# Optimization experiments

Measured on AMD Instinct MI355X. Metric: run time of the kernel, lower is better.

## Reference

```python
import jax, jax.numpy as jnp
import numpy as np

B, C_IN, T_IN = 128, 128, 2500
C_OUT, K, STRIDE, PAD = 64, 27, 4, 13  # T_out = 625
BN_EPS = 1e-5
SURROGATE_ALPHA = 4.0


def binarize_weight(w):
    """1-bit (XNOR-Net style) weight quantization with straight-through estimator.
    w: (O, I, K). Per-output-channel scale = mean |w|."""
    alpha = jnp.mean(jnp.abs(w), axis=(1, 2), keepdims=True)
    wq = jnp.sign(w) * alpha
    return w + jax.lax.stop_gradient(wq - w)


def spike(x):
    """Heaviside spike with sigmoid surrogate gradient (STE)."""
    hard = (x > 0).astype(x.dtype)
    soft = jax.nn.sigmoid(SURROGATE_ALPHA * x)
    return soft + jax.lax.stop_gradient(hard - soft)


def setup_inputs() -> dict:
    key = jax.random.key(0)
    ks = jax.random.split(key, 8)
    scale_conv = 1.0 / np.sqrt(C_IN * K)
    scale_lin = 1.0 / np.sqrt(C_OUT)
    return {
        "x": jax.random.normal(ks[0], (B, C_IN, T_IN), dtype=jnp.float32),
        "conv_w": jax.random.normal(ks[1], (C_OUT, C_IN, K), dtype=jnp.float32) * scale_conv,
        "conv_b": jnp.zeros((C_OUT,), dtype=jnp.float32),
        "bn_gamma": jnp.ones((C_OUT,), dtype=jnp.float32),
        "bn_beta": jnp.zeros((C_OUT,), dtype=jnp.float32),
        "bn_mean": jax.random.normal(ks[2], (C_OUT,), dtype=jnp.float32) * 0.1,
        "bn_var": jax.random.uniform(ks[3], (C_OUT,), dtype=jnp.float32, minval=0.5, maxval=1.5),
        "wq": jax.random.normal(ks[4], (C_OUT, C_OUT), dtype=jnp.float32) * scale_lin,
        "wk": jax.random.normal(ks[5], (C_OUT, C_OUT), dtype=jnp.float32) * scale_lin,
        "wv": jax.random.normal(ks[6], (C_OUT, C_OUT), dtype=jnp.float32) * scale_lin,
        "wo": jax.random.normal(ks[7], (C_OUT, C_OUT), dtype=jnp.float32) * scale_lin,
    }


def reference(x, conv_w, conv_b, bn_gamma, bn_beta, bn_mean, bn_var, wq, wk, wv, wo):
    # --- 1-bit quantized conv1d, stride 4 ---
    w_bin = binarize_weight(conv_w)
    y = jax.lax.conv_general_dilated(
        x, w_bin, window_strides=(STRIDE,), padding=[(PAD, PAD)],
        dimension_numbers=("NCH", "OIH", "NCH"))
    y = y + conv_b[None, :, None]  # (B, C_OUT, 625)

    # --- BatchNorm1d (inference stats) + ELU ---
    inv = jax.lax.rsqrt(bn_var + BN_EPS)
    y = (y - bn_mean[None, :, None]) * (inv * bn_gamma)[None, :, None] + bn_beta[None, :, None]
    y = jax.nn.elu(y)

    # --- Global spiking attention (single head) ---
    s = spike(y)                                   # (B, C, T) binary spikes
    q = jnp.einsum("oc,bct->bot", wq, s)           # (B, C, T)
    k = jnp.einsum("oc,bct->bot", wk, s)
    v = jnp.einsum("oc,bct->bot", wv, y)
    scores = jnp.einsum("bct,bcs->bts", q, k) / jnp.sqrt(jnp.asarray(C_OUT, y.dtype))
    attn = jax.nn.softmax(scores, axis=-1)         # (B, T, T)
    ctx = jnp.einsum("bts,bcs->bct", attn, v)      # (B, C, T)
    out = y + jnp.einsum("oc,bct->bot", wo, ctx)   # residual
    return out
```

## Files before the change

### kernel.cpp

```cpp
#include <hip/hip_runtime.h>
#include <math.h>

#define B_    128
#define CIN   128
#define TIN   2500
#define COUT  64
#define KW    27
#define TOUT  625
#define TPAD  640
#define CTT   32
#define GROWS 152

typedef __bf16 bf16x8 __attribute__((ext_vector_type(8)));
typedef float  f32x4  __attribute__((ext_vector_type(4)));

__device__ __forceinline__ unsigned short f32_to_bf16_rne(float v) {
    unsigned u = __float_as_uint(v);
    u += 0x7FFFu + ((u >> 16) & 1u);
    return (unsigned short)(u >> 16);
}

__device__ __forceinline__ f32x4 mfma_bf16(bf16x8 a, bf16x8 b, f32x4 c) {
    return __builtin_amdgcn_mfma_f32_16x16x32_bf16(a, b, c, 0, 0, 0);
}

__global__ void binarize_kernel(const float* __restrict__ w,
                                unsigned* __restrict__ sgn2,
                                float* __restrict__ alpha_out) {
    int o = blockIdx.x, tid = threadIdx.x;
    __shared__ float red[256];
    const float* wo_ = w + (size_t)o * (CIN * KW);
    float s = 0.f;
    for (int idx = tid; idx < CIN * KW; idx += 256) s += fabsf(wo_[idx]);
    red[tid] = s;
    __syncthreads();
    for (int st = 128; st > 0; st >>= 1) {
        if (tid < st) red[tid] += red[tid + st];
        __syncthreads();
    }
    if (tid == 0) alpha_out[o] = red[0] / (float)(CIN * KW);

    for (int t = tid; t < KW * 4; t += 256) {
        int kk = t >> 2, kg = t & 3;
        unsigned u = 0;
#pragma unroll
        for (int cs = 0; cs < 4; cs++) {
#pragma unroll
            for (int j = 0; j < 8; j++) {
                int c = cs * 32 + kg * 8 + j;
                float v = wo_[c * KW + kk];
                unsigned bit = (v > 0.f) ? 0u : 1u;
                u |= bit << (cs * 8 + j);
            }
        }
        sgn2[(kk * 4 + kg) * 64 + o] = u;
    }
}

__global__ void transpose_w_kernel(const float* __restrict__ wq, const float* __restrict__ wk,
                                   const float* __restrict__ wv, const float* __restrict__ wo,
                                   const float* __restrict__ conv_b, const float* __restrict__ gamma_,
                                   const float* __restrict__ beta_, const float* __restrict__ mean_,
                                   const float* __restrict__ var_, const float* __restrict__ alpha_,
                                   unsigned short* __restrict__ w3_h, unsigned short* __restrict__ w3_l,
                                   unsigned short* __restrict__ wo_h, unsigned short* __restrict__ wo_l,
                                   float* __restrict__ scA, float* __restrict__ scB) {
    if (blockIdx.x < 3) {
        const float* srcs[3] = {wq, wk, wv};
        const float* src = srcs[blockIdx.x];
        unsigned short* dh = w3_h + (size_t)blockIdx.x * 4096;
        unsigned short* dl = w3_l + (size_t)blockIdx.x * 4096;
        for (int idx = threadIdx.x; idx < 4096; idx += 256) {
            float v = src[idx];
            unsigned short h = f32_to_bf16_rne(v);
            float hf = __uint_as_float((unsigned)h << 16);
            dh[idx] = h;
            dl[idx] = f32_to_bf16_rne(v - hf);
        }
    } else if (blockIdx.x == 3) {
        for (int idx = threadIdx.x; idx < 4096; idx += 256) {
            float v = wo[idx];
            unsigned short h = f32_to_bf16_rne(v);
            float hf = __uint_as_float((unsigned)h << 16);
            wo_h[idx] = h;
            wo_l[idx] = f32_to_bf16_rne(v - hf);
        }
    } else {
        int o = threadIdx.x;
        if (o < 64) {
            float inv = rsqrtf(var_[o] + 1e-5f);
            float G = gamma_[o] * inv;
            scA[o] = alpha_[o] * G;
            scB[o] = (conv_b[o] - mean_[o]) * G + beta_[o];
        }
    }
}

__global__ __launch_bounds__(256, 4) void conv_kernel(
    const float* __restrict__ x, const unsigned* __restrict__ sgn2,
    const float* __restrict__ scA, const float* __restrict__ scB,
    const unsigned short* __restrict__ w3_h, const unsigned short* __restrict__ w3_l,
    float* __restrict__ y_out,
    unsigned short* __restrict__ q_h, unsigned short* __restrict__ k_h,
    unsigned short* __restrict__ vT_h)
{
    __shared__ __align__(16) unsigned short xhi[GROWS * 128];
    __shared__ __align__(16) unsigned long long sgnlut[16];
    unsigned short* y_sh = xhi;
    unsigned short* s_sh = xhi + 2048;
    unsigned short* q_sh = xhi + 4096;
    unsigned short* k_sh = xhi + 6144;
    unsigned short* v_sh = xhi + 8192;

    int b = blockIdx.y;
    int t0 = blockIdx.x * CTT;
    int tid = threadIdx.x;

    if (tid < 16) {
        unsigned long long e = 0;
#pragma unroll
        for (int j = 0; j < 4; ++j) {
            unsigned long long h = ((tid >> j) & 1) ? 0xBF80ull : 0x3F80ull;
            e |= h << (16 * j);
        }
        sgnlut[tid] = e;
    }

    const float* xb = x + (size_t)b * CIN * TIN;
    int gbase = 4 * t0 - 13;
    for (int task = tid; task < 16 * GROWS; task += 256) {
        int c8 = task / GROWS, gl = task - c8 * GROWS;
        int g = gbase + gl;
        bool valid = (gl < 151) && ((unsigned)g < (unsigned)TIN);
        float vs[8];
#pragma unroll
        for (int j = 0; j < 8; j++)
            vs[j] = valid ? xb[(size_t)(c8 * 8 + j) * TIN + g] : 0.f;
        union { unsigned u[4]; uint4 q; } H;
#pragma unroll
        for (int j = 0; j < 4; j++) {
            unsigned short h0 = f32_to_bf16_rne(vs[2 * j]);
            unsigned short h1 = f32_to_bf16_rne(vs[2 * j + 1]);
            H.u[j] = (unsigned)h0 | ((unsigned)h1 << 16);
        }
        int c8p = c8 ^ ((gl >> 2) & 15);
        *(uint4*)(xhi + gl * 128 + c8p * 8) = H.q;
    }
    __syncthreads();

    int wave = tid >> 6, lane = tid & 63;
    int o0 = wave * 16;
    int n = lane & 15, kg = lane >> 4;

    f32x4 acc0 = {0.f, 0.f, 0.f, 0.f};
    f32x4 acc1 = {0.f, 0.f, 0.f, 0.f};

    const unsigned* sgb = sgn2 + (size_t)kg * 64 + o0 + n;
    unsigned sa = sgb[0];

#pragma unroll 1
    for (int kk = 0; kk < KW; ++kk) {
        unsigned na = 0;
        if (kk < KW - 1) na = sgb[(kk + 1) * 256];
        int gl = 4 * n + kk;
        int rot = (gl >> 2) & 15;
        const unsigned short* xr0 = xhi + gl * 128;
        const unsigned short* xr1 = xr0 + 8192;
#pragma unroll
        for (int cs = 0; cs < 4; ++cs) {
            int c8p = (cs * 4 + kg) ^ rot;
            bf16x8 b0 = *(const bf16x8*)(xr0 + c8p * 8);
            bf16x8 b1 = *(const bf16x8*)(xr1 + c8p * 8);
            unsigned byte = (sa >> (8 * cs)) & 0xFFu;
            union { unsigned long long u[2]; bf16x8 v; } A;
            A.u[0] = sgnlut[byte & 15u];
            A.u[1] = sgnlut[byte >> 4];
            acc0 = mfma_bf16(A.v, b0, acc0);
            acc1 = mfma_bf16(A.v, b1, acc1);
        }
        sa = na;
    }

    int quad = kg, col = n;
    unsigned long long ypk[2], spk[2];
#pragma unroll
    for (int tt = 0; tt < 2; ++tt) {
        int t_g = t0 + tt * 16 + col;
        f32x4 a = tt ? acc1 : acc0;
        unsigned long long yp = 0, sp = 0;
#pragma unroll
        for (int r = 0; r < 4; ++r) {
            int o = o0 + quad * 4 + r;
            float s = a[r] * scA[o] + scB[o];
            float yv = s > 0.f ? s : expm1f(s);
            if (t_g < TOUT) {
                y_out[((size_t)b * COUT + o) * TOUT + t_g] = yv;
                yp |= (unsigned long long)f32_to_bf16_rne(yv) << (16 * r);
                if (yv > 0.f) sp |= 0x3F80ull << (16 * r);
            }
        }
        ypk[tt] = yp; spk[tt] = sp;
    }
    __syncthreads();

    int c8w = (o0 >> 3) + (quad >> 1);
    int cof = (quad & 1) * 4;
#pragma unroll
    for (int tt = 0; tt < 2; ++tt) {
        int tl = tt * 16 + col;
        int idx = tl * 64 + ((c8w ^ (tl & 7)) << 3) + cof;
        *(unsigned long long*)(y_sh + idx) = ypk[tt];
        *(unsigned long long*)(s_sh + idx) = spk[tt];
    }
    __syncthreads();

    bf16x8 sf[2][2], yf[2][2];
#pragma unroll
    for (int tt = 0; tt < 2; ++tt)
#pragma unroll
        for (int ks = 0; ks < 2; ++ks) {
            int tl = tt * 16 + col;
            int idx = tl * 64 + (((ks * 4 + quad) ^ (tl & 7)) << 3);
            sf[tt][ks] = *(const bf16x8*)(s_sh + idx);
            yf[tt][ks] = *(const bf16x8*)(y_sh + idx);
        }
    size_t wofs = (size_t)(o0 + col) * 64 + quad * 8;
    f32x4 qa[2], ka[2], va[2];
#pragma unroll
    for (int tt = 0; tt < 2; ++tt) {
        qa[tt] = (f32x4){0.f, 0.f, 0.f, 0.f};
        ka[tt] = (f32x4){0.f, 0.f, 0.f, 0.f};
        va[tt] = (f32x4){0.f, 0.f, 0.f, 0.f};
    }
#pragma unroll
    for (int ks = 0; ks < 2; ++ks) {
        bf16x8 aqh = *(const bf16x8*)(w3_h + wofs + ks * 32);
        bf16x8 aql = *(const bf16x8*)(w3_l + wofs + ks * 32);
        bf16x8 akh = *(const bf16x8*)(w3_h + 4096 + wofs + ks * 32);
        bf16x8 akl = *(const bf16x8*)(w3_l + 4096 + wofs + ks * 32);
        bf16x8 avh = *(const bf16x8*)(w3_h + 8192 + wofs + ks * 32);
        bf16x8 avl = *(const bf16x8*)(w3_l + 8192 + wofs + ks * 32);
#pragma unroll
        for (int tt = 0; tt < 2; ++tt) {
            qa[tt] = mfma_bf16(aqh, sf[tt][ks], qa[tt]);
            qa[tt] = mfma_bf16(aql, sf[tt][ks], qa[tt]);
            ka[tt] = mfma_bf16(akh, sf[tt][ks], ka[tt]);
            ka[tt] = mfma_bf16(akl, sf[tt][ks], ka[tt]);
            va[tt] = mfma_bf16(avh, yf[tt][ks], va[tt]);
            va[tt] = mfma_bf16(avl, yf[tt][ks], va[tt]);
        }
    }
#pragma unroll
    for (int tt = 0; tt < 2; ++tt) {
        int tl = tt * 16 + col;
        int idx = tl * 64 + ((c8w ^ (tl & 7)) << 3) + cof;
        unsigned long long qp = 0, kp = 0;
#pragma unroll
        for (int r = 0; r < 4; ++r) {
            qp |= (unsigned long long)f32_to_bf16_rne(qa[tt][r]) << (16 * r);
            kp |= (unsigned long long)f32_to_bf16_rne(ka[tt][r]) << (16 * r);
        }
        *(unsigned long long*)(q_sh + idx) = qp;
        *(unsigned long long*)(k_sh + idx) = kp;
#pragma unroll
        for (int r = 0; r < 4; ++r) {
            int c = o0 + quad * 4 + r;
            int vidx = c * 32 + (((tt * 2 + (col >> 3)) ^ quad) << 3) + (col & 7);
            v_sh[vidx] = f32_to_bf16_rne(va[tt][r]);
        }
    }
    __syncthreads();

    {
        int tl = tid >> 3, seg = tid & 7;
        int idx = tl * 64 + ((seg ^ (tl & 7)) << 3);
        uint4 qv = *(const uint4*)(q_sh + idx);
        uint4 kv = *(const uint4*)(k_sh + idx);
        size_t go = ((size_t)b * TPAD + t0 + tl) * 64 + seg * 8;
        *(uint4*)(q_h + go) = qv;
        *(uint4*)(k_h + go) = kv;
        int c = tid >> 2, ts = tid & 3;
        int vidx = c * 32 + ((ts ^ ((c >> 2) & 3)) << 3);
        uint4 vv = *(const uint4*)(v_sh + vidx);
        *(uint4*)(vT_h + ((size_t)b * 64 + c) * TPAD + t0 + ts * 8) = vv;
    }
}

__global__ __launch_bounds__(512, 3) void attn_kernel(
    const unsigned short* __restrict__ q_h, const unsigned short* __restrict__ k_h,
    const unsigned short* __restrict__ vT_h, const float* __restrict__ y,
    const unsigned short* __restrict__ wo_h, const unsigned short* __restrict__ wo_l,
    float* __restrict__ out)
{
    __shared__ __align__(16) float sc_sh[16 * 648];
    __shared__ float ctx_sh[2 * 64 * 17];
    __shared__ float rden[16];

    int b = blockIdx.y, t0 = blockIdx.x * 16, tid = threadIdx.x;
    int wave = tid >> 6, lane = tid & 63;
    int quad = lane >> 4, nlo = lane & 15;

    const unsigned short* qb = q_h + ((size_t)b * TPAD + t0 + nlo) * 64 + quad * 8;
    bf16x8 qa0 = *(const bf16x8*)(qb);
    bf16x8 qa1 = *(const bf16x8*)(qb + 32);
    const unsigned short* kbase = k_h + (size_t)b * TPAD * 64 + quad * 8;
#pragma unroll 5
    for (int nt = 0; nt < 5; ++nt) {
        int s = wave * 80 + nt * 16 + nlo;
        const unsigned short* krow = kbase + (size_t)s * 64;
        bf16x8 kb0 = *(const bf16x8*)(krow);
        bf16x8 kb1 = *(const bf16x8*)(krow + 32);
        f32x4 acc = {0.f, 0.f, 0.f, 0.f};
        acc = mfma_bf16(qa0, kb0, acc);
        acc = mfma_bf16(qa1, kb1, acc);
#pragma unroll
        for (int r = 0; r < 4; ++r)
            sc_sh[(quad * 4 + r) * 648 + s] = acc[r] * 0.125f;
    }
    __syncthreads();

    int ti1 = tid >> 5, sg = tid & 31;
    float* srow = &sc_sh[ti1 * 648];
    float mx = -3.0e38f;
    for (int s = sg; s < TOUT; s += 32) mx = fmaxf(mx, srow[s]);
#pragma unroll
    for (int off = 16; off >= 1; off >>= 1) mx = fmaxf(mx, __shfl_xor(mx, off));

    unsigned short* prow = (unsigned short*)srow;
    float sum = 0.f;
#pragma unroll
    for (int k2 = 0; k2 < 10; ++k2) {
        int s = 2 * sg + 64 * k2;
        float2 v2 = *(const float2*)(srow + s);
        float e0 = (s     < TOUT) ? __expf(v2.x - mx) : 0.f;
        float e1 = (s + 1 < TOUT) ? __expf(v2.y - mx) : 0.f;
        sum += e0 + e1;
        unsigned u0 = __float_as_uint(e0); u0 += 0x7FFFu + ((u0 >> 16) & 1u);
        unsigned u1 = __float_as_uint(e1); u1 += 0x7FFFu + ((u1 >> 16) & 1u);
        *(unsigned*)(prow + s) = (u0 >> 16) | (u1 & 0xFFFF0000u);
    }
#pragma unroll
    for (int off = 16; off >= 1; off >>= 1) sum += __shfl_xor(sum, off);
    if (sg == 0) rden[ti1] = 1.f / sum;
    __syncthreads();

    int cw = (wave & 3) * 16, kh = wave >> 2;
    const unsigned short* vb = vT_h + ((size_t)b * 64 + cw + nlo) * TPAD;
    const unsigned short* pb = (const unsigned short*)sc_sh + nlo * 1296;
    f32x4 cacc = {0.f, 0.f, 0.f, 0.f};
    int ks0 = kh * 10;
#pragma unroll 5
    for (int i = 0; i < 10; ++i) {
        int ks = ks0 + i;
        bf16x8 pv = *(const bf16x8*)(pb + ks * 32 + quad * 8);
        bf16x8 v8 = *(const bf16x8*)(vb + ks * 32 + quad * 8);
        cacc = mfma_bf16(pv, v8, cacc);
    }
#pragma unroll
    for (int r = 0; r < 4; ++r)
        ctx_sh[kh * 1088 + (cw + nlo) * 17 + quad * 4 + r] = cacc[r] * rden[quad * 4 + r];
    __syncthreads();

    if (wave < 4) {
        const unsigned short* woh = wo_h + (size_t)(wave * 16 + nlo) * 64 + quad * 8;
        const unsigned short* wol = wo_l + (size_t)(wave * 16 + nlo) * 64 + quad * 8;
        f32x4 oacc = {0.f, 0.f, 0.f, 0.f};
#pragma unroll
        for (int ks = 0; ks < 2; ++ks) {
            union { unsigned short u[8]; bf16x8 v; } Bc;
#pragma unroll
            for (int j = 0; j < 8; ++j) {
                int c = ks * 32 + quad * 8 + j;
                float cv = ctx_sh[c * 17 + nlo] + ctx_sh[1088 + c * 17 + nlo];
                Bc.u[j] = f32_to_bf16_rne(cv);
            }
            bf16x8 ah = *(const bf16x8*)(woh + ks * 32);
            bf16x8 al = *(const bf16x8*)(wol + ks * 32);
            oacc = mfma_bf16(ah, Bc.v, oacc);
            oacc = mfma_bf16(al, Bc.v, oacc);
        }
        int t_g = t0 + nlo;
        if (t_g < TOUT) {
#pragma unroll
            for (int r = 0; r < 4; ++r) {
                int o = wave * 16 + quad * 4 + r;
                size_t off = ((size_t)b * COUT + o) * TOUT + t_g;
                out[off] = y[off] + oacc[r];
            }
        }
    }
}

extern "C" void kernel_launch(void* const* d_in, const int* in_sizes, int n_in,
                              void* d_out, int out_size, void* d_ws, size_t ws_size,
                              hipStream_t stream) {
    const float* x        = (const float*)d_in[0];
    const float* conv_w   = (const float*)d_in[1];
    const float* conv_b   = (const float*)d_in[2];
    const float* bn_gamma = (const float*)d_in[3];
    const float* bn_beta  = (const float*)d_in[4];
    const float* bn_mean  = (const float*)d_in[5];
    const float* bn_var   = (const float*)d_in[6];
    const float* wq       = (const float*)d_in[7];
    const float* wk       = (const float*)d_in[8];
    const float* wv       = (const float*)d_in[9];
    const float* wo       = (const float*)d_in[10];
    float* out = (float*)d_out;
    float* ws  = (float*)d_ws;

    unsigned* sgn2        = (unsigned*)ws;
    float* alpha          = ws + 110592;
    float* scA            = ws + 110656;
    float* scB            = ws + 110720;
    unsigned short* w3_h  = (unsigned short*)(ws + 110848);
    unsigned short* w3_l  = (unsigned short*)(ws + 116992);
    unsigned short* wo_h  = (unsigned short*)(ws + 123136);
    unsigned short* wo_l  = (unsigned short*)(ws + 125184);
    float* yb             = ws + 131072;
    unsigned short* q_h   = (unsigned short*)(ws + 5251072);
    unsigned short* k_h   = (unsigned short*)(ws + 7872512);
    unsigned short* vT_h  = (unsigned short*)(ws + 10493952);

    hipLaunchKernelGGL(binarize_kernel, dim3(64), dim3(256), 0, stream, conv_w, sgn2, alpha);
    hipLaunchKernelGGL(transpose_w_kernel, dim3(5), dim3(256), 0, stream,
                       wq, wk, wv, wo, conv_b, bn_gamma, bn_beta, bn_mean, bn_var, alpha,
                       w3_h, w3_l, wo_h, wo_l, scA, scB);
    hipLaunchKernelGGL(conv_kernel, dim3(20, 128), dim3(256), 0, stream,
                       x, sgn2, scA, scB, w3_h, w3_l, yb, q_h, k_h, vT_h);
    hipLaunchKernelGGL(attn_kernel, dim3(40, 128), dim3(512), 0, stream,
                       q_h, k_h, vT_h, yb, wo_h, wo_l, out);
}
```

Baseline: 433.0 us.

## Merge prep kernels, use 32x32 MFMA conv with split-K, remap blocks for XCD locality

Merges the binarize and weight-transpose kernels into one prep kernel, removing a launch and the alpha round trip through memory. The conv kernel now uses 32x32x16 bf16 MFMA, with the channel dimension split across wave pairs and partial sums reduced through shared memory. Both conv and attention blocks get a swizzled block-id mapping (id&7 stride) so neighbouring tiles of the same batch land on the same XCD for cache locality. This adds an extra LDS reduction and barrier in the conv epilogue, and leaves half the waves idle during it.

```diff
diff --git a/kernel.cpp b/kernel.cpp
--- a/kernel.cpp
+++ b/kernel.cpp
@@ -13,6 +13,7 @@
 
 typedef __bf16 bf16x8 __attribute__((ext_vector_type(8)));
 typedef float  f32x4  __attribute__((ext_vector_type(4)));
+typedef float  f32x16 __attribute__((ext_vector_type(16)));
 
 __device__ __forceinline__ unsigned short f32_to_bf16_rne(float v) {
     unsigned u = __float_as_uint(v);
@@ -24,74 +25,69 @@
     return __builtin_amdgcn_mfma_f32_16x16x32_bf16(a, b, c, 0, 0, 0);
 }
 
-__global__ void binarize_kernel(const float* __restrict__ w,
-                                unsigned* __restrict__ sgn2,
-                                float* __restrict__ alpha_out) {
-    int o = blockIdx.x, tid = threadIdx.x;
-    __shared__ float red[256];
-    const float* wo_ = w + (size_t)o * (CIN * KW);
-    float s = 0.f;
-    for (int idx = tid; idx < CIN * KW; idx += 256) s += fabsf(wo_[idx]);
-    red[tid] = s;
-    __syncthreads();
-    for (int st = 128; st > 0; st >>= 1) {
-        if (tid < st) red[tid] += red[tid + st];
+__global__ void prep_kernel(const float* __restrict__ w,
+                            const float* __restrict__ wq, const float* __restrict__ wk,
+                            const float* __restrict__ wv, const float* __restrict__ wo,
+                            const float* __restrict__ conv_b, const float* __restrict__ gamma_,
+                            const float* __restrict__ beta_, const float* __restrict__ mean_,
+                            const float* __restrict__ var_,
+                            unsigned* __restrict__ sgn2,
+                            unsigned short* __restrict__ w3_h, unsigned short* __restrict__ w3_l,
+                            unsigned short* __restrict__ wo_h, unsigned short* __restrict__ wo_l,
+                            float* __restrict__ scA, float* __restrict__ scB) {
+    int blk = blockIdx.x, tid = threadIdx.x;
+    if (blk < 64) {
+        __shared__ float red[256];
+        const float* wrow = w + (size_t)blk * (CIN * KW);
+        float s = 0.f;
+        for (int idx = tid; idx < CIN * KW; idx += 256) s += fabsf(wrow[idx]);
+        red[tid] = s;
         __syncthreads();
-    }
-    if (tid == 0) alpha_out[o] = red[0] / (float)(CIN * KW);
-
-    for (int t = tid; t < KW * 4; t += 256) {
-        int kk = t >> 2, kg = t & 3;
-        unsigned u = 0;
-#pragma unroll
-        for (int cs = 0; cs < 4; cs++) {
-#pragma unroll
-            for (int j = 0; j < 8; j++) {
-                int c = cs * 32 + kg * 8 + j;
-                float v = wo_[c * KW + kk];
-                unsigned bit = (v > 0.f) ? 0u : 1u;
-                u |= bit << (cs * 8 + j);
+        for (int st = 128; st > 0; st >>= 1) {
+            if (tid < st) red[tid] += red[tid + st];
+            __syncthreads();
+        }
+        if (tid == 0) {
+            float alpha = red[0] / (float)(CIN * KW);
+            float inv = rsqrtf(var_[blk] + 1e-5f);
+            float G = gamma_[blk] * inv;
+            scA[blk] = alpha * G;
+            scB[blk] = (conv_b[blk] - mean_[blk]) * G + beta_[blk];
+        }
+        for (int t = tid; t < KW * 4; t += 256) {
+            int kk = t >> 2, kg = t & 3;
+            unsigned u = 0;
+#pragma unroll
+            for (int cs = 0; cs < 4; cs++) {
+#pragma unroll
+                for (int j = 0; j < 8; j++) {
+                    int c = cs * 32 + kg * 8 + j;
+                    float v = wrow[c * KW + kk];
+                    unsigned bit = (v > 0.f) ? 0u : 1u;
+                    u |= bit << (cs * 8 + j);
+                }
             }
-        }
-        sgn2[(kk * 4 + kg) * 64 + o] = u;
-    }
-}
-
-__global__ void transpose_w_kernel(const float* __restrict__ wq, const float* __restrict__ wk,
-                                   const float* __restrict__ wv, const float* __restrict__ wo,
-                                   const float* __restrict__ conv_b, const float* __restrict__ gamma_,
-                                   const float* __restrict__ beta_, const float* __restrict__ mean_,
-                                   const float* __restrict__ var_, const float* __restrict__ alpha_,
-                                   unsigned short* __restrict__ w3_h, unsigned short* __restrict__ w3_l,
-                                   unsigned short* __restrict__ wo_h, unsigned short* __restrict__ wo_l,
-                                   float* __restrict__ scA, float* __restrict__ scB) {
-    if (blockIdx.x < 3) {
+            sgn2[(kk * 4 + kg) * 64 + blk] = u;
+        }
+    } else if (blk < 67) {
         const float* srcs[3] = {wq, wk, wv};
-        const float* src = srcs[blockIdx.x];
-        unsigned short* dh = w3_h + (size_t)blockIdx.x * 4096;
-        unsigned short* dl = w3_l + (size_t)blockIdx.x * 4096;
-        for (int idx = threadIdx.x; idx < 4096; idx += 256) {
+        const float* src = srcs[blk - 64];
+        unsigned short* dh = w3_h + (size_t)(blk - 64) * 4096;
+        unsigned short* dl = w3_l + (size_t)(blk - 64) * 4096;
+        for (int idx = tid; idx < 4096; idx += 256) {
             float v = src[idx];
             unsigned short h = f32_to_bf16_rne(v);
             float hf = __uint_as_float((unsigned)h << 16);
             dh[idx] = h;
             dl[idx] = f32_to_bf16_rne(v - hf);
         }
-    } else if (blockIdx.x == 3) {
-        for (int idx = threadIdx.x; idx < 4096; idx += 256) {
+    } else {
+        for (int idx = tid; idx < 4096; idx += 256) {
             float v = wo[idx];
             unsigned short h = f32_to_bf16_rne(v);
             float hf = __uint_as_float((unsigned)h << 16);
             wo_h[idx] = h;
             wo_l[idx] = f32_to_bf16_rne(v - hf);
-        }
-    } else {
-        int o = threadIdx.x;
-        if (o < 64) {
-            float inv = rsqrtf(var_[o] + 1e-5f);
-            float G = gamma_[o] * inv;
-            scA[o] = alpha_[o] * G;
-            scB[o] = (conv_b[o] - mean_[o]) * G + beta_[o];
         }
     }
 }
@@ -111,10 +107,13 @@
     unsigned short* q_sh = xhi + 4096;
     unsigned short* k_sh = xhi + 6144;
     unsigned short* v_sh = xhi + 8192;
-
-    int b = blockIdx.y;
-    int t0 = blockIdx.x * CTT;
+    float* part_sh = (float*)(xhi + 10240);
+
     int tid = threadIdx.x;
+    int id = blockIdx.x + 20 * blockIdx.y;
+    int nid = (id & 7) * 320 + (id >> 3);
+    int b = nid / 20;
+    int t0 = (nid - b * 20) * CTT;
 
     if (tid < 16) {
         unsigned long long e = 0;
@@ -149,71 +148,79 @@
     __syncthreads();
 
     int wave = tid >> 6, lane = tid & 63;
-    int o0 = wave * 16;
-    int n = lane & 15, kg = lane >> 4;
-
-    f32x4 acc0 = {0.f, 0.f, 0.f, 0.f};
-    f32x4 acc1 = {0.f, 0.f, 0.f, 0.f};
-
-    const unsigned* sgb = sgn2 + (size_t)kg * 64 + o0 + n;
-    unsigned sa = sgb[0];
+    int oh = wave & 1, ch = wave >> 1;
+    int o0w = oh * 32;
+    int lo = lane & 31;
+    int kg1 = lane >> 5;
+
+    f32x16 acc = {0.f};
+    const unsigned* sgb = sgn2 + o0w + lo;
+    unsigned w0 = sgb[kg1 * 64];
+    unsigned w1 = sgb[(kg1 + 2) * 64];
 
 #pragma unroll 1
     for (int kk = 0; kk < KW; ++kk) {
-        unsigned na = 0;
-        if (kk < KW - 1) na = sgb[(kk + 1) * 256];
-        int gl = 4 * n + kk;
+        unsigned n0 = 0, n1 = 0;
+        if (kk < KW - 1) {
+            n0 = sgb[((kk + 1) * 4 + kg1) * 64];
+            n1 = sgb[((kk + 1) * 4 + kg1 + 2) * 64];
+        }
+        int gl = 4 * lo + kk;
         int rot = (gl >> 2) & 15;
-        const unsigned short* xr0 = xhi + gl * 128;
-        const unsigned short* xr1 = xr0 + 8192;
-#pragma unroll
-        for (int cs = 0; cs < 4; ++cs) {
-            int c8p = (cs * 4 + kg) ^ rot;
-            bf16x8 b0 = *(const bf16x8*)(xr0 + c8p * 8);
-            bf16x8 b1 = *(const bf16x8*)(xr1 + c8p * 8);
-            unsigned byte = (sa >> (8 * cs)) & 0xFFu;
+        const unsigned short* xr = xhi + gl * 128;
+#pragma unroll
+        for (int ks = 0; ks < 4; ++ks) {
+            int oct = ch * 8 + ks * 2 + kg1;
+            int c8p = oct ^ rot;
+            bf16x8 bx = *(const bf16x8*)(xr + c8p * 8);
+            unsigned wsel = (ks & 1) ? w1 : w0;
+            unsigned byte = (wsel >> (8 * (ch * 2 + (ks >> 1)))) & 0xFFu;
             union { unsigned long long u[2]; bf16x8 v; } A;
             A.u[0] = sgnlut[byte & 15u];
             A.u[1] = sgnlut[byte >> 4];
-            acc0 = mfma_bf16(A.v, b0, acc0);
-            acc1 = mfma_bf16(A.v, b1, acc1);
-        }
-        sa = na;
-    }
-
-    int quad = kg, col = n;
-    unsigned long long ypk[2], spk[2];
-#pragma unroll
-    for (int tt = 0; tt < 2; ++tt) {
-        int t_g = t0 + tt * 16 + col;
-        f32x4 a = tt ? acc1 : acc0;
-        unsigned long long yp = 0, sp = 0;
-#pragma unroll
-        for (int r = 0; r < 4; ++r) {
-            int o = o0 + quad * 4 + r;
-            float s = a[r] * scA[o] + scB[o];
-            float yv = s > 0.f ? s : expm1f(s);
-            if (t_g < TOUT) {
-                y_out[((size_t)b * COUT + o) * TOUT + t_g] = yv;
-                yp |= (unsigned long long)f32_to_bf16_rne(yv) << (16 * r);
-                if (yv > 0.f) sp |= 0x3F80ull << (16 * r);
+            acc = __builtin_amdgcn_mfma_f32_32x32x16_bf16(A.v, bx, acc, 0, 0, 0);
+        }
+        w0 = n0; w1 = n1;
+    }
+    __syncthreads();
+
+    if (ch == 1) {
+        float* p = part_sh + oh * 1024 + lane;
+#pragma unroll
+        for (int r = 0; r < 16; ++r) p[r * 64] = acc[r];
+    }
+    __syncthreads();
+
+    if (ch == 0) {
+        const float* p = part_sh + oh * 1024 + lane;
+        int t_g = t0 + lo;
+        bool tv = t_g < TOUT;
+#pragma unroll
+        for (int g2 = 0; g2 < 4; ++g2) {
+            unsigned long long yp = 0, sp = 0;
+#pragma unroll
+            for (int j = 0; j < 4; ++j) {
+                int r = g2 * 4 + j;
+                float v = acc[r] + p[r * 64];
+                int o = o0w + 4 * kg1 + 8 * g2 + j;
+                float s = v * scA[o] + scB[o];
+                float yv = s > 0.f ? s : expm1f(s);
+                if (tv) {
+                    y_out[((size_t)b * COUT + o) * TOUT + t_g] = yv;
+                    yp |= (unsigned long long)f32_to_bf16_rne(yv) << (16 * j);
+                    if (yv > 0.f) sp |= 0x3F80ull << (16 * j);
+                }
             }
-        }
-        ypk[tt] = yp; spk[tt] = sp;
-    }
-    __syncthreads();
-
-    int c8w = (o0 >> 3) + (quad >> 1);
-    int cof = (quad & 1) * 4;
-#pragma unroll
-    for (int tt = 0; tt < 2; ++tt) {
-        int tl = tt * 16 + col;
-        int idx = tl * 64 + ((c8w ^ (tl & 7)) << 3) + cof;
-        *(unsigned long long*)(y_sh + idx) = ypk[tt];
-        *(unsigned long long*)(s_sh + idx) = spk[tt];
-    }
-    __syncthreads();
-
+            int c8 = 4 * oh + g2;
+            int idx = lo * 64 + ((c8 ^ (lo & 7)) << 3) + 4 * kg1;
+            *(unsigned long long*)(y_sh + idx) = yp;
+            *(unsigned long long*)(s_sh + idx) = sp;
+        }
+    }
+    __syncthreads();
+
+    int quad = lane >> 4, col = lane & 15;
+    int o0 = wave * 16;
     bf16x8 sf[2][2], yf[2][2];
 #pragma unroll
     for (int tt = 0; tt < 2; ++tt)
@@ -250,6 +257,8 @@
             va[tt] = mfma_bf16(avl, yf[tt][ks], va[tt]);
         }
     }
+    int c8w = (o0 >> 3) + (quad >> 1);
+    int cof = (quad & 1) * 4;
 #pragma unroll
     for (int tt = 0; tt < 2; ++tt) {
         int tl = tt * 16 + col;
@@ -296,7 +305,12 @@
     __shared__ float ctx_sh[2 * 64 * 17];
     __shared__ float rden[16];
 
-    int b = blockIdx.y, t0 = blockIdx.x * 16, tid = threadIdx.x;
+    int tid = threadIdx.x;
+    int id = blockIdx.x + 40 * blockIdx.y;
+    int nid = (id & 7) * 640 + (id >> 3);
+    int b = nid / 40;
+    int t0 = (nid - b * 40) * 16;
+
     int wave = tid >> 6, lane = tid & 63;
     int quad = lane >> 4, nlo = lane & 15;
 
@@ -409,7 +423,6 @@
     float* ws  = (float*)d_ws;
 
     unsigned* sgn2        = (unsigned*)ws;
-    float* alpha          = ws + 110592;
     float* scA            = ws + 110656;
     float* scB            = ws + 110720;
     unsigned short* w3_h  = (unsigned short*)(ws + 110848);
@@ -421,10 +434,9 @@
     unsigned short* k_h   = (unsigned short*)(ws + 7872512);
     unsigned short* vT_h  = (unsigned short*)(ws + 10493952);
 
-    hipLaunchKernelGGL(binarize_kernel, dim3(64), dim3(256), 0, stream, conv_w, sgn2, alpha);
-    hipLaunchKernelGGL(transpose_w_kernel, dim3(5), dim3(256), 0, stream,
-                       wq, wk, wv, wo, conv_b, bn_gamma, bn_beta, bn_mean, bn_var, alpha,
-                       w3_h, w3_l, wo_h, wo_l, scA, scB);
+    hipLaunchKernelGGL(prep_kernel, dim3(68), dim3(256), 0, stream,
+                       conv_w, wq, wk, wv, wo, conv_b, bn_gamma, bn_beta, bn_mean, bn_var,
+                       sgn2, w3_h, w3_l, wo_h, wo_l, scA, scB);
     hipLaunchKernelGGL(conv_kernel, dim3(20, 128), dim3(256), 0, stream,
                        x, sgn2, scA, scB, w3_h, w3_l, yb, q_h, k_h, vT_h);
     hipLaunchKernelGGL(attn_kernel, dim3(40, 128), dim3(512), 0, stream,
```

Result: no change. 427.0 us (-1.4%).
